# Kernel tuning notes

Hardware: AMD Instinct MI355X
Metric: run time of the kernel (lower is better)

## Reference

```python
import jax, jax.numpy as jnp
import numpy as np

N_EVENTS = 4_000_000
HW = 128          # DVS sensor resolution
TICKS = 10_000    # simulation horizon
KH, KW = 3, 3     # kernel_size
OUT_CH = 64       # out_channels


def setup_inputs() -> dict:
    key = jax.random.key(0)
    k1, k2, k3 = jax.random.split(key, 3)
    return {
        "values": jnp.ones((N_EVENTS,), dtype=jnp.float32),            # spike value 1.0 per add_spike
        "ticks_in": jax.random.randint(k1, (N_EVENTS,), 0, TICKS, dtype=jnp.int32),
        "xs": jax.random.randint(k2, (N_EVENTS,), 0, HW, dtype=jnp.int32),
        "ys": jax.random.randint(k3, (N_EVENTS,), 0, HW, dtype=jnp.int32),
        "stride": 1,
    }


def reference(values, ticks_in, xs, ys, stride):
    """Event-driven spike routing of Conv2dT.forward.

    Returns the per-channel synapse input buffers [OUT_CH, KH*KW, TICKS]:
    buffer[c, s, t] = total spike value scattered into synapse s of soma c at tick t.
    (The subsequent izh-soma ODE simulation lives in the external ABM model.)
    """
    S = KH * KW
    off_y = jnp.repeat(jnp.arange(KH), KW)   # [S], ky per synapse_idx = ky*KW + kx
    off_x = jnp.tile(jnp.arange(KW), KH)     # [S], kx per synapse_idx

    out_x = xs[None, :] - off_x[:, None]     # [S, N]
    out_y = ys[None, :] - off_y[:, None]     # [S, N]
    valid = (out_x >= 0) & (out_y >= 0) & (out_x % stride == 0) & (out_y % stride == 0)
    contrib = jnp.where(valid, values[None, :], jnp.zeros((), values.dtype))  # [S, N]

    # scatter-add over ticks for each synapse offset
    buf = jnp.zeros((S, TICKS), dtype=values.dtype)
    buf = buf.at[jnp.arange(S)[:, None], ticks_in[None, :]].add(contrib)     # [S, T]

    # every output channel receives the identical spike dispatch
    return jnp.broadcast_to(buf[None], (OUT_CH, S, TICKS))
```

## Files before the change

kernel.cpp:

```cpp
#include <hip/hip_runtime.h>

#define TICKS 10000
#define NSYN 9
#define OUT_CH 64

#define SCATTER_BLOCKS 512
#define SCATTER_THREADS 1024

__global__ void zero_kernel(float* __restrict__ p, int n) {
    int i = blockIdx.x * blockDim.x + threadIdx.x;
    if (i < n) p[i] = 0.0f;
}

__global__ __launch_bounds__(SCATTER_THREADS) void scatter_kernel(
    const float* __restrict__ values,
    const int*   __restrict__ ticks,
    const int*   __restrict__ xs,
    const int*   __restrict__ ys,
    const int*   __restrict__ stride_p,
    float*       __restrict__ hist,
    int n)
{
    __shared__ float lhist[TICKS];
    const int stride = stride_p[0];
    const int tid = threadIdx.x;

    if (stride == 1) {
        for (int j = tid; j < TICKS; j += SCATTER_THREADS) lhist[j] = 0.0f;
        __syncthreads();

        const int n4  = n >> 2;
        const int gsz = gridDim.x * SCATTER_THREADS;
        const float4* __restrict__ v4 = (const float4*)values;
        const int4*   __restrict__ t4 = (const int4*)ticks;
        const int4*   __restrict__ x4 = (const int4*)xs;
        const int4*   __restrict__ y4 = (const int4*)ys;

        for (int i = blockIdx.x * SCATTER_THREADS + tid; i < n4; i += gsz) {
            float4 v = v4[i];
            int4   t = t4[i];
            int4   x = x4[i];
            int4   y = y4[i];

            if (x.x >= 2 && y.x >= 2) atomicAdd(&lhist[t.x], v.x);
            else atomicAdd(&hist[(min(y.x, 2) * 3 + min(x.x, 2)) * TICKS + t.x], v.x);

            if (x.y >= 2 && y.y >= 2) atomicAdd(&lhist[t.y], v.y);
            else atomicAdd(&hist[(min(y.y, 2) * 3 + min(x.y, 2)) * TICKS + t.y], v.y);

            if (x.z >= 2 && y.z >= 2) atomicAdd(&lhist[t.z], v.z);
            else atomicAdd(&hist[(min(y.z, 2) * 3 + min(x.z, 2)) * TICKS + t.z], v.z);

            if (x.w >= 2 && y.w >= 2) atomicAdd(&lhist[t.w], v.w);
            else atomicAdd(&hist[(min(y.w, 2) * 3 + min(x.w, 2)) * TICKS + t.w], v.w);
        }

        if ((n & 3) && blockIdx.x == 0 && tid == 0) {
            for (int i = n4 << 2; i < n; ++i) {
                atomicAdd(&hist[(min(ys[i], 2) * 3 + min(xs[i], 2)) * TICKS + ticks[i]],
                          values[i]);
            }
        }

        __syncthreads();

        int phase = (blockIdx.x * 157) % TICKS;
        for (int j = tid; j < TICKS; j += SCATTER_THREADS) {
            int b = j + phase;
            if (b >= TICKS) b -= TICKS;
            float v = lhist[b];
            if (v != 0.0f) atomicAdd(&hist[8 * TICKS + b], v);
        }
    } else {
        const int gsz = gridDim.x * SCATTER_THREADS;
        for (int i = blockIdx.x * SCATTER_THREADS + tid; i < n; i += gsz) {
            float v = values[i];
            int   t = ticks[i];
            int   x = xs[i];
            int   y = ys[i];
            #pragma unroll
            for (int ky = 0; ky < 3; ++ky) {
                int oy = y - ky;
                if (oy < 0 || (oy % stride) != 0) continue;
                #pragma unroll
                for (int kx = 0; kx < 3; ++kx) {
                    int ox = x - kx;
                    if (ox < 0 || (ox % stride) != 0) continue;
                    atomicAdd(&hist[(ky * 3 + kx) * TICKS + t], v);
                }
            }
        }
    }
}

__global__ __launch_bounds__(256) void emit_kernel(
    const float* __restrict__ hist,
    const int*   __restrict__ stride_p,
    float*       __restrict__ out)
{
    int t = blockIdx.x * blockDim.x + threadIdx.x;
    if (t >= TICKS) return;
    const int stride = stride_p[0];

    float b[NSYN];
    #pragma unroll
    for (int s = 0; s < NSYN; ++s) b[s] = hist[s * TICKS + t];

    if (stride == 1) {
        #pragma unroll
        for (int r = 0; r < 3; ++r) {
            b[r * 3 + 1] += b[r * 3 + 2];
            b[r * 3 + 0] += b[r * 3 + 1];
        }
        #pragma unroll
        for (int c = 0; c < 3; ++c) {
            b[3 + c] += b[6 + c];
            b[0 + c] += b[3 + c];
        }
    }

    for (int c = blockIdx.y; c < OUT_CH; c += gridDim.y) {
        #pragma unroll
        for (int s = 0; s < NSYN; ++s) {
            out[(c * NSYN + s) * TICKS + t] = b[s];
        }
    }
}

extern "C" void kernel_launch(void* const* d_in, const int* in_sizes, int n_in,
                              void* d_out, int out_size, void* d_ws, size_t ws_size,
                              hipStream_t stream) {
    const float* values   = (const float*)d_in[0];
    const int*   ticks    = (const int*)  d_in[1];
    const int*   xs       = (const int*)  d_in[2];
    const int*   ys       = (const int*)  d_in[3];
    const int*   stride_p = (const int*)  d_in[4];
    float*       out      = (float*)      d_out;
    const int n = in_sizes[0];

    const size_t hist_bytes = (size_t)NSYN * TICKS * sizeof(float);
    float* hist;
    bool hist_in_out;
    if (ws_size >= hist_bytes) {
        hist = (float*)d_ws;
        hist_in_out = false;
    } else {
        hist = out;
        hist_in_out = true;
    }

    {
        int nh = NSYN * TICKS;
        zero_kernel<<<(nh + 255) / 256, 256, 0, stream>>>(hist, nh);
    }

    scatter_kernel<<<SCATTER_BLOCKS, SCATTER_THREADS, 0, stream>>>(
        values, ticks, xs, ys, stride_p, hist, n);

    {
        dim3 grid((TICKS + 255) / 256, hist_in_out ? 1 : 64);
        emit_kernel<<<grid, 256, 0, stream>>>(hist, stride_p, out);
    }
}
```

Baseline: 147.9 us.

## Spread per-block histogram flush over partial buffers and vectorize output broadcast

Each scatter block now flushes its shared-memory histogram into one of 32 partial global buffers instead of all 512 blocks atomically adding into a single row. The goal is to cut atomic contention on the flush. A new combine kernel sums the partials and applies the stride-1 prefix sums. The emit kernel then writes the 64-channel broadcast with float4 stores. This costs one extra kernel launch, more workspace to zero, and a 32-way read in the combine step.

After: 146.7 us. No clear change (-0.8%).

```diff
diff --git a/kernel.cpp b/kernel.cpp
--- a/kernel.cpp
+++ b/kernel.cpp
@@ -4,6 +4,7 @@
 #define NSYN 9
 #define OUT_CH 64
 
+#define NPART 32
 #define SCATTER_BLOCKS 512
 #define SCATTER_THREADS 1024
 
@@ -18,7 +19,9 @@
     const int*   __restrict__ xs,
     const int*   __restrict__ ys,
     const int*   __restrict__ stride_p,
-    float*       __restrict__ hist,
+    float*       __restrict__ buf,
+    float*       __restrict__ part,
+    int P,
     int n)
 {
     __shared__ float lhist[TICKS];
@@ -43,33 +46,35 @@
             int4   y = y4[i];
 
             if (x.x >= 2 && y.x >= 2) atomicAdd(&lhist[t.x], v.x);
-            else atomicAdd(&hist[(min(y.x, 2) * 3 + min(x.x, 2)) * TICKS + t.x], v.x);
+            else atomicAdd(&buf[(min(y.x, 2) * 3 + min(x.x, 2)) * TICKS + t.x], v.x);
 
             if (x.y >= 2 && y.y >= 2) atomicAdd(&lhist[t.y], v.y);
-            else atomicAdd(&hist[(min(y.y, 2) * 3 + min(x.y, 2)) * TICKS + t.y], v.y);
+            else atomicAdd(&buf[(min(y.y, 2) * 3 + min(x.y, 2)) * TICKS + t.y], v.y);
 
             if (x.z >= 2 && y.z >= 2) atomicAdd(&lhist[t.z], v.z);
-            else atomicAdd(&hist[(min(y.z, 2) * 3 + min(x.z, 2)) * TICKS + t.z], v.z);
+            else atomicAdd(&buf[(min(y.z, 2) * 3 + min(x.z, 2)) * TICKS + t.z], v.z);
 
             if (x.w >= 2 && y.w >= 2) atomicAdd(&lhist[t.w], v.w);
-            else atomicAdd(&hist[(min(y.w, 2) * 3 + min(x.w, 2)) * TICKS + t.w], v.w);
+            else atomicAdd(&buf[(min(y.w, 2) * 3 + min(x.w, 2)) * TICKS + t.w], v.w);
         }
 
         if ((n & 3) && blockIdx.x == 0 && tid == 0) {
             for (int i = n4 << 2; i < n; ++i) {
-                atomicAdd(&hist[(min(ys[i], 2) * 3 + min(xs[i], 2)) * TICKS + ticks[i]],
-                          values[i]);
+                int cls = min(ys[i], 2) * 3 + min(xs[i], 2);
+                if (cls == 8) atomicAdd(&part[ticks[i]], values[i]);
+                else          atomicAdd(&buf[cls * TICKS + ticks[i]], values[i]);
             }
         }
 
         __syncthreads();
 
-        int phase = (blockIdx.x * 157) % TICKS;
+        float* __restrict__ dst = part + (size_t)(blockIdx.x % P) * TICKS;
+        int phase = ((blockIdx.x / P) * 613) % TICKS;
         for (int j = tid; j < TICKS; j += SCATTER_THREADS) {
             int b = j + phase;
             if (b >= TICKS) b -= TICKS;
             float v = lhist[b];
-            if (v != 0.0f) atomicAdd(&hist[8 * TICKS + b], v);
+            if (v != 0.0f) atomicAdd(&dst[b], v);
         }
     } else {
         const int gsz = gridDim.x * SCATTER_THREADS;
@@ -86,17 +91,18 @@
                 for (int kx = 0; kx < 3; ++kx) {
                     int ox = x - kx;
                     if (ox < 0 || (ox % stride) != 0) continue;
-                    atomicAdd(&hist[(ky * 3 + kx) * TICKS + t], v);
+                    atomicAdd(&buf[(ky * 3 + kx) * TICKS + t], v);
                 }
             }
         }
     }
 }
 
-__global__ __launch_bounds__(256) void emit_kernel(
-    const float* __restrict__ hist,
+__global__ __launch_bounds__(256) void combine_kernel(
+    float*       __restrict__ buf,
+    const float* __restrict__ part,
     const int*   __restrict__ stride_p,
-    float*       __restrict__ out)
+    int P)
 {
     int t = blockIdx.x * blockDim.x + threadIdx.x;
     if (t >= TICKS) return;
@@ -104,9 +110,12 @@
 
     float b[NSYN];
     #pragma unroll
-    for (int s = 0; s < NSYN; ++s) b[s] = hist[s * TICKS + t];
+    for (int s = 0; s < NSYN; ++s) b[s] = buf[s * TICKS + t];
 
     if (stride == 1) {
+        float s8 = 0.0f;
+        for (int p = 0; p < P; ++p) s8 += part[(size_t)p * TICKS + t];
+        b[8] = s8;
         #pragma unroll
         for (int r = 0; r < 3; ++r) {
             b[r * 3 + 1] += b[r * 3 + 2];
@@ -119,10 +128,29 @@
         }
     }
 
+    #pragma unroll
+    for (int s = 0; s < NSYN; ++s) buf[s * TICKS + t] = b[s];
+}
+
+__global__ __launch_bounds__(256) void emit_kernel(
+    const float* __restrict__ buf,
+    float*       __restrict__ out)
+{
+    const int T4 = TICKS / 4;
+    int t = blockIdx.x * blockDim.x + threadIdx.x;
+    if (t >= T4) return;
+
+    const float4* __restrict__ b4 = (const float4*)buf;
+    float4*       __restrict__ o4 = (float4*)out;
+
+    float4 b[NSYN];
+    #pragma unroll
+    for (int s = 0; s < NSYN; ++s) b[s] = b4[s * T4 + t];
+
     for (int c = blockIdx.y; c < OUT_CH; c += gridDim.y) {
         #pragma unroll
         for (int s = 0; s < NSYN; ++s) {
-            out[(c * NSYN + s) * TICKS + t] = b[s];
+            o4[(c * NSYN + s) * T4 + t] = b[s];
         }
     }
 }
@@ -138,27 +166,35 @@
     float*       out      = (float*)      d_out;
     const int n = in_sizes[0];
 
-    const size_t hist_bytes = (size_t)NSYN * TICKS * sizeof(float);
-    float* hist;
-    bool hist_in_out;
-    if (ws_size >= hist_bytes) {
-        hist = (float*)d_ws;
-        hist_in_out = false;
+    const size_t need = (size_t)(NSYN + NPART) * TICKS * sizeof(float);
+    float* buf;
+    float* part;
+    int    P;
+    bool   fallback;
+    if (ws_size >= need) {
+        buf = (float*)d_ws;
+        part = buf + (size_t)NSYN * TICKS;
+        P = NPART;
+        fallback = false;
     } else {
-        hist = out;
-        hist_in_out = true;
+        buf = out;
+        part = buf + (size_t)8 * TICKS;
+        P = 1;
+        fallback = true;
     }
 
     {
-        int nh = NSYN * TICKS;
-        zero_kernel<<<(nh + 255) / 256, 256, 0, stream>>>(hist, nh);
+        int nz = (fallback ? NSYN : (NSYN + NPART)) * TICKS;
+        zero_kernel<<<(nz + 255) / 256, 256, 0, stream>>>(buf, nz);
     }
 
     scatter_kernel<<<SCATTER_BLOCKS, SCATTER_THREADS, 0, stream>>>(
-        values, ticks, xs, ys, stride_p, hist, n);
+        values, ticks, xs, ys, stride_p, buf, part, P, n);
+
+    combine_kernel<<<(TICKS + 255) / 256, 256, 0, stream>>>(buf, part, stride_p, P);
 
     {
-        dim3 grid((TICKS + 255) / 256, hist_in_out ? 1 : 64);
-        emit_kernel<<<grid, 256, 0, stream>>>(hist, stride_p, out);
-    }
-}
+        dim3 grid((TICKS / 4 + 255) / 256, fallback ? 1 : 64);
+        emit_kernel<<<grid, 256, 0, stream>>>(buf, out);
+    }
+}
```
